# Kernel tuning notes

Measured on AMD Instinct MI355X. Metric: run time of the kernel, lower is better.

Reference implementation:

```python
import jax, jax.numpy as jnp
import numpy as np

TOP_K = 2
NUM_EXPERTS = 8
LB_COEFF = 0.01


def setup_inputs() -> dict:
    key = jax.random.key(0)
    ks = jax.random.split(key, 5)
    B, S, D, F, E = 4, 2048, 1024, 4096, NUM_EXPERTS
    s_in = 0.02
    return {
        "x": jax.random.normal(ks[0], (B, S, D), jnp.float32),
        "gate_w": jax.random.normal(ks[1], (D, E), jnp.float32) * s_in,
        "gate_b": jnp.zeros((E,), jnp.float32),
        "fc1_w": jax.random.normal(ks[2], (E, D, 2 * F), jnp.float32) * s_in,
        "fc1_b": jnp.zeros((E, 2 * F), jnp.float32),
        "fc2_w": jax.random.normal(ks[3], (E, F, D), jnp.float32) * s_in,
        "fc2_b": jnp.zeros((E, D), jnp.float32),
    }


def reference(x, gate_w, gate_b, fc1_w, fc1_b, fc2_w, fc2_b):
    B, S, D = x.shape
    E = gate_w.shape[1]
    xt = x.reshape(-1, D)                      # [T, D]
    T = xt.shape[0]

    gate_logits = xt @ gate_w + gate_b        # [T, E]
    gate_probs = jax.nn.softmax(gate_logits, axis=-1)
    top_w, top_i = jax.lax.top_k(gate_probs, TOP_K)      # [T, K]
    w_norm = top_w / (top_w.sum(-1, keepdims=True) + 1e-6)

    rows = jnp.arange(T)[:, None]
    # per-token per-expert combine weight (0 if expert not in top-k)
    combine = jnp.zeros((T, E), xt.dtype).at[rows, top_i].add(w_norm)  # [T, E]

    out = jnp.zeros_like(xt)
    for e in range(E):  # fixed small expert loop; each is a dense GEMM
        h = xt @ fc1_w[e] + fc1_b[e]                      # [T, 2F]
        a, g = jnp.split(h, 2, axis=-1)
        act = a * jax.nn.gelu(g, approximate=False)       # SwiGLU (exact gelu, torch default)
        y = act @ fc2_w[e] + fc2_b[e]                     # [T, D]
        out = out + combine[:, e:e + 1] * y

    chosen_mask = jnp.zeros((T, E), gate_probs.dtype).at[rows, top_i].set(1.0)
    frac = chosen_mask.mean(0)
    mean_probs = gate_probs.mean(0)
    lb_loss = LB_COEFF * E * jnp.sum(frac * mean_probs)

    return out.reshape(B, S, D), lb_loss
```

## Files before the change

### kernel.cpp

```cpp
#include <hip/hip_runtime.h>
#include <hip/hip_bf16.h>
#include <stdint.h>

typedef __attribute__((ext_vector_type(4))) float f32x4;
typedef __attribute__((ext_vector_type(16))) float f32x16;
typedef __attribute__((ext_vector_type(8))) __bf16 bf16x8;
typedef __attribute__((ext_vector_type(4))) unsigned short u16x4;
typedef unsigned short u16;

#define NTOK 8192
#define DDIM 1024
#define FDIM 4096
#define NEXP 8
#define NT1 144

#define WS_XB    0ull
#define WS_W1T   (16777216ull)
#define WS_W2T   (WS_W1T + 134217728ull)
#define WS_ACT   (WS_W2T + 67108864ull)
#define WS_LIST  (WS_ACT + 142606336ull)
#define WS_PAIRW (WS_LIST + 262144ull)
#define WS_CNT   (WS_PAIRW + 262144ull)
#define WS_SUMP  (WS_CNT + 32ull)
#define WS_PAD   (WS_SUMP + 32ull)
#define WS_OFF   (WS_PAD + 32ull)
#define WS_T1E   (WS_OFF + 32ull)
#define WS_T1R   (WS_T1E + 1024ull)
#define WS_SE    (WS_T1R + 1024ull)
#define WS_SP    (WS_SE + 65536ull)

static __device__ __forceinline__ u16 bf16rne(float f) {
  union { float f; uint32_t u; } c; c.f = f;
  return (u16)((c.u + 0x7FFFu + ((c.u >> 16) & 1u)) >> 16);
}

static __device__ __forceinline__ void load_lds16(const void* g, void* l) {
  __builtin_amdgcn_global_load_lds((const __attribute__((address_space(1))) void*)g,
                                   (__attribute__((address_space(3))) void*)l, 16, 0, 0);
}

__global__ __launch_bounds__(256) void gate_kernel(
    const float* __restrict__ x, const float* __restrict__ gw,
    const float* __restrict__ gb, u16* __restrict__ xb,
    int* __restrict__ cnt, float* __restrict__ sump,
    int* __restrict__ list, float* __restrict__ pairw,
    int* __restrict__ slotE, int* __restrict__ slotP) {
  const int tid = threadIdx.x;
  const int lane = tid & 63;
  const int wv = tid >> 6;
  const int t = blockIdx.x * 4 + wv;

  __shared__ float sp[8];
  if (tid < 8) sp[tid] = 0.f;
  __syncthreads();

  float acc[8] = {0.f,0.f,0.f,0.f,0.f,0.f,0.f,0.f};
  const float4* x4 = (const float4*)x + (size_t)t * 256;
  u16x4* xb4 = (u16x4*)xb + (size_t)t * 256;
  #pragma unroll
  for (int it = 0; it < 4; ++it) {
    const float4 xv = x4[it * 64 + lane];
    u16x4 bv;
    bv[0] = bf16rne(xv.x); bv[1] = bf16rne(xv.y);
    bv[2] = bf16rne(xv.z); bv[3] = bf16rne(xv.w);
    xb4[it * 64 + lane] = bv;
    const int d0 = (it * 64 + lane) * 4;
    #pragma unroll
    for (int j = 0; j < 4; ++j) {
      const float xs = (j == 0) ? xv.x : ((j == 1) ? xv.y : ((j == 2) ? xv.z : xv.w));
      const float* g = gw + (size_t)(d0 + j) * 8;
      #pragma unroll
      for (int e2 = 0; e2 < 8; ++e2) acc[e2] += xs * g[e2];
    }
  }
  #pragma unroll
  for (int e2 = 0; e2 < 8; ++e2) {
    float v = acc[e2];
    v += __shfl_xor(v, 1);  v += __shfl_xor(v, 2);  v += __shfl_xor(v, 4);
    v += __shfl_xor(v, 8);  v += __shfl_xor(v, 16); v += __shfl_xor(v, 32);
    acc[e2] = v;
  }
  float p[8]; float mx = -1e30f;
  #pragma unroll
  for (int e2 = 0; e2 < 8; ++e2) { p[e2] = acc[e2] + gb[e2]; mx = fmaxf(mx, p[e2]); }
  float s = 0.f;
  #pragma unroll
  for (int e2 = 0; e2 < 8; ++e2) { p[e2] = expf(p[e2] - mx); s += p[e2]; }
  const float inv = 1.f / s;
  #pragma unroll
  for (int e2 = 0; e2 < 8; ++e2) p[e2] *= inv;

  if (lane == 0) {
    int i1 = 0; float v1 = p[0];
    #pragma unroll
    for (int e2 = 1; e2 < 8; ++e2) if (p[e2] > v1) { v1 = p[e2]; i1 = e2; }
    int i2 = 0; float v2 = -1.f;
    #pragma unroll
    for (int e2 = 0; e2 < 8; ++e2) if (e2 != i1 && p[e2] > v2) { v2 = p[e2]; i2 = e2; }
    const float den = v1 + v2 + 1e-6f;
    const int p1 = atomicAdd(&cnt[i1], 1);
    list[i1 * NTOK + p1] = t; pairw[i1 * NTOK + p1] = v1 / den;
    slotE[2 * t] = i1; slotP[2 * t] = p1;
    const int p2 = atomicAdd(&cnt[i2], 1);
    list[i2 * NTOK + p2] = t; pairw[i2 * NTOK + p2] = v2 / den;
    slotE[2 * t + 1] = i2; slotP[2 * t + 1] = p2;
    #pragma unroll
    for (int e2 = 0; e2 < 8; ++e2) atomicAdd(&sp[e2], p[e2]);
  }
  __syncthreads();
  if (tid < 8) atomicAdd(&sump[tid], sp[tid]);
}

__global__ __launch_bounds__(256) void conv_transpose(
    const float* __restrict__ in, u16* __restrict__ out, int R, int C) {
  __shared__ float tile[64][65];
  const int e = blockIdx.z;
  const float* pin = in + (size_t)e * R * C;
  u16* pout = out + (size_t)e * R * C;
  const int tx = threadIdx.x & 15;
  const int ty = threadIdx.x >> 4;
  const int c0 = blockIdx.x * 64;
  const int r0 = blockIdx.y * 64;
  #pragma unroll
  for (int i = 0; i < 4; ++i) {
    const int r = ty + i * 16;
    const float4 v = *(const float4*)(pin + (size_t)(r0 + r) * C + c0 + tx * 4);
    tile[r][tx * 4 + 0] = v.x;
    tile[r][tx * 4 + 1] = v.y;
    tile[r][tx * 4 + 2] = v.z;
    tile[r][tx * 4 + 3] = v.w;
  }
  __syncthreads();
  #pragma unroll
  for (int i = 0; i < 4; ++i) {
    const int c = ty + i * 16;
    u16x4 o;
    o[0] = bf16rne(tile[tx * 4 + 0][c]);
    o[1] = bf16rne(tile[tx * 4 + 1][c]);
    o[2] = bf16rne(tile[tx * 4 + 2][c]);
    o[3] = bf16rne(tile[tx * 4 + 3][c]);
    *(u16x4*)(pout + (size_t)(c0 + c) * R + r0 + tx * 4) = o;
  }
}

__global__ void route_finalize(const int* __restrict__ cnt, const float* __restrict__ sump,
                               int* __restrict__ padc, int* __restrict__ offs,
                               int* __restrict__ list, float* __restrict__ pairw,
                               int* __restrict__ t1e, int* __restrict__ t1r,
                               float* __restrict__ lb_out) {
  __shared__ int s_c[8], s_p[8];
  const int tid = threadIdx.x;
  if (tid == 0) {
    int o = 0; float lb = 0.f;
    for (int e = 0; e < 8; ++e) {
      const int c = cnt[e];
      const int pc = (c + 127) & ~127;
      s_c[e] = c; s_p[e] = pc;
      padc[e] = pc; offs[e] = o; o += pc;
      lb += ((float)c / 8192.f) * (sump[e] / 8192.f);
    }
    lb_out[0] = 0.01f * 8.f * lb;
    int n1 = 0;
    for (int e = 0; e < 8; ++e)
      for (int r = 0; r < s_p[e]; r += 128) { t1e[n1] = e; t1r[n1] = r; ++n1; }
    for (; n1 < NT1; ++n1) { t1e[n1] = -1; t1r[n1] = 0; }
  }
  __syncthreads();
  for (int e = 0; e < 8; ++e)
    for (int pq = s_c[e] + tid; pq < s_p[e]; pq += blockDim.x) {
      list[e * NTOK + pq] = 0; pairw[e * NTOK + pq] = 0.f;
    }
}

__global__ __launch_bounds__(256) void gemm1_kernel(
    const u16* __restrict__ xb, const u16* __restrict__ w1t,
    const float* __restrict__ b1, const int* __restrict__ list,
    const int* __restrict__ offs,
    const int* __restrict__ t1e, const int* __restrict__ t1r,
    u16* __restrict__ act) {
  const int tt = blockIdx.y;
  const int e = t1e[tt];
  if (e < 0) return;
  const int row0 = t1r[tt];
  const int j = blockIdx.x;
  const int off_e = offs[e];

  __shared__ u16 lds[16384];

  const int tid = threadIdx.x;
  const int lane = tid & 63;
  const int wv = tid >> 6;
  const int wr = wv >> 1, wc = wv & 1;
  const int l31 = lane & 31, s5 = lane >> 5;

  const int rt = tid >> 2;
  const int ce = ((tid & 3) ^ ((rt >> 1) & 3)) * 8;
  const int tok0 = list[e * NTOK + row0 + rt];
  const int tok1 = list[e * NTOK + row0 + rt + 64];
  const u16* srcA0 = xb + (size_t)tok0 * DDIM + ce;
  const u16* srcA1 = xb + (size_t)tok1 * DDIM + ce;
  const int rB1 = rt + 64;
  const int gn0 = j * 64 + ((rt >> 6) & 1) * 32 + (rt & 31) + ((rt >> 5) & 1) * FDIM;
  const int gn1 = j * 64 + ((rB1 >> 6) & 1) * 32 + (rB1 & 31) + ((rB1 >> 5) & 1) * FDIM;
  const u16* srcB0 = w1t + ((size_t)e * 2 * FDIM + gn0) * DDIM + ce;
  const u16* srcB1 = w1t + ((size_t)e * 2 * FDIM + gn1) * DDIM + ce;

  const int xsw = (l31 >> 1) & 3;
  const int kel0 = (s5 ^ xsw) * 8;
  const int aB0 = (wr * 64 + l31) * 32 + kel0;  const int aB1 = aB0 ^ 16;
  const int bB0 = (wc * 64 + l31) * 32 + kel0;  const int bB1 = bB0 ^ 16;

  f32x16 acc[2][2];
  #pragma unroll
  for (int m = 0; m < 2; ++m)
    #pragma unroll
    for (int n = 0; n < 2; ++n)
      #pragma unroll
      for (int i = 0; i < 16; ++i) acc[m][n][i] = 0.f;

  #define STAGE1(buf, kt) do { \
    u16* _dA = &lds[(buf) * 4096 + wv * 512]; \
    u16* _dB = &lds[8192 + (buf) * 4096 + wv * 512]; \
    load_lds16(srcA0 + (kt) * 32, _dA); \
    load_lds16(srcA1 + (kt) * 32, _dA + 2048); \
    load_lds16(srcB0 + (kt) * 32, _dB); \
    load_lds16(srcB1 + (kt) * 32, _dB + 2048); \
  } while (0)

  STAGE1(0, 0);
  for (int kt = 0; kt < DDIM / 32; ++kt) {
    const int cur = kt & 1;
    __syncthreads();
    if (kt + 1 < DDIM / 32) STAGE1(cur ^ 1, kt + 1);
    const int bA = cur * 4096;
    const int bB = 8192 + cur * 4096;
    bf16x8 a0[2], a1[2], Bh0[2], Bh1[2];
    #pragma unroll
    for (int m = 0; m < 2; ++m) {
      a0[m] = *(const bf16x8*)&lds[bA + aB0 + m * 1024];
      a1[m] = *(const bf16x8*)&lds[bA + aB1 + m * 1024];
    }
    #pragma unroll
    for (int n = 0; n < 2; ++n) {
      Bh0[n] = *(const bf16x8*)&lds[bB + bB0 + n * 1024];
      Bh1[n] = *(const bf16x8*)&lds[bB + bB1 + n * 1024];
    }
    #pragma unroll
    for (int m = 0; m < 2; ++m)
      #pragma unroll
      for (int n = 0; n < 2; ++n) {
        acc[m][n] = __builtin_amdgcn_mfma_f32_32x32x16_bf16(a0[m], Bh0[n], acc[m][n], 0, 0, 0);
        acc[m][n] = __builtin_amdgcn_mfma_f32_32x32x16_bf16(a1[m], Bh1[n], acc[m][n], 0, 0, 0);
      }
  }
  #undef STAGE1

  const size_t actrow0 = (size_t)(off_e + row0);
  const int col = j * 64 + wc * 32 + l31;
  const float ba = b1[e * (2 * FDIM) + col];
  const float bg = b1[e * (2 * FDIM) + FDIM + col];
  #pragma unroll
  for (int m = 0; m < 2; ++m) {
    #pragma unroll
    for (int r = 0; r < 16; ++r) {
      const int row = wr * 64 + m * 32 + (r & 3) + 8 * (r >> 2) + 4 * s5;
      const float a = acc[m][0][r] + ba;
      const float g = acc[m][1][r] + bg;
      const float u2 = 1.5957691216057308f * (g + 0.044715f * g * g * g);
      const float sg = 1.f / (1.f + __expf(-u2));
      act[(actrow0 + row) * FDIM + col] = bf16rne(a * g * sg);
    }
  }
}

__global__ __launch_bounds__(256) void gemm2_kernel(
    const u16* __restrict__ act, const u16* __restrict__ w2t,
    const float* __restrict__ b2, const float* __restrict__ pairw,
    const int* __restrict__ offs,
    const int* __restrict__ t1e, const int* __restrict__ t1r,
    float* __restrict__ y) {
  const int bid = blockIdx.x;
  const int r8 = bid & 7;
  const int q = bid >> 3;
  const int jt = q & 7;
  const int tt = (q >> 3) * 8 + r8;
  const int e = t1e[tt];
  if (e < 0) return;
  const int row0 = t1r[tt];
  const int off_e = offs[e];

  __shared__ u16 lds[16384];

  const int tid = threadIdx.x;
  const int lane = tid & 63;
  const int wv = tid >> 6;
  const int wr = wv >> 1, wc = wv & 1;
  const int l31 = lane & 31, s5 = lane >> 5;

  const int rt = tid >> 2;
  const int ce = ((tid & 3) ^ ((rt >> 1) & 3)) * 8;
  const u16* srcA0 = act + (size_t)(off_e + row0 + rt) * FDIM + ce;
  const u16* srcA1 = act + (size_t)(off_e + row0 + rt + 64) * FDIM + ce;
  const u16* srcB0 = w2t + ((size_t)e * DDIM + jt * 128 + rt) * FDIM + ce;
  const u16* srcB1 = w2t + ((size_t)e * DDIM + jt * 128 + rt + 64) * FDIM + ce;

  const int xsw = (l31 >> 1) & 3;
  const int kel0 = (s5 ^ xsw) * 8;
  const int aB0 = (wr * 64 + l31) * 32 + kel0;  const int aB1 = aB0 ^ 16;
  const int bB0 = (wc * 64 + l31) * 32 + kel0;  const int bB1 = bB0 ^ 16;

  f32x16 acc[2][2];
  #pragma unroll
  for (int m = 0; m < 2; ++m)
    #pragma unroll
    for (int n = 0; n < 2; ++n)
      #pragma unroll
      for (int i = 0; i < 16; ++i) acc[m][n][i] = 0.f;

  #define STAGE2(buf, kt) do { \
    u16* _dA = &lds[(buf) * 4096 + wv * 512]; \
    u16* _dB = &lds[8192 + (buf) * 4096 + wv * 512]; \
    load_lds16(srcA0 + (kt) * 32, _dA); \
    load_lds16(srcA1 + (kt) * 32, _dA + 2048); \
    load_lds16(srcB0 + (kt) * 32, _dB); \
    load_lds16(srcB1 + (kt) * 32, _dB + 2048); \
  } while (0)

  STAGE2(0, 0);
  for (int kt = 0; kt < FDIM / 32; ++kt) {
    const int cur = kt & 1;
    __syncthreads();
    if (kt + 1 < FDIM / 32) STAGE2(cur ^ 1, kt + 1);
    const int bA = cur * 4096;
    const int bB = 8192 + cur * 4096;
    bf16x8 a0[2], a1[2], Bh0[2], Bh1[2];
    #pragma unroll
    for (int m = 0; m < 2; ++m) {
      a0[m] = *(const bf16x8*)&lds[bA + aB0 + m * 1024];
      a1[m] = *(const bf16x8*)&lds[bA + aB1 + m * 1024];
    }
    #pragma unroll
    for (int n = 0; n < 2; ++n) {
      Bh0[n] = *(const bf16x8*)&lds[bB + bB0 + n * 1024];
      Bh1[n] = *(const bf16x8*)&lds[bB + bB1 + n * 1024];
    }
    #pragma unroll
    for (int m = 0; m < 2; ++m)
      #pragma unroll
      for (int n = 0; n < 2; ++n) {
        acc[m][n] = __builtin_amdgcn_mfma_f32_32x32x16_bf16(a0[m], Bh0[n], acc[m][n], 0, 0, 0);
        acc[m][n] = __builtin_amdgcn_mfma_f32_32x32x16_bf16(a1[m], Bh1[n], acc[m][n], 0, 0, 0);
      }
  }
  #undef STAGE2

  #pragma unroll
  for (int m = 0; m < 2; ++m) {
    #pragma unroll
    for (int r = 0; r < 16; ++r) {
      const int row = wr * 64 + m * 32 + (r & 3) + 8 * (r >> 2) + 4 * s5;
      const int pos = row0 + row;
      const float pw = pairw[e * NTOK + pos];
      if (pw != 0.f) {
        float* yr = y + (size_t)(off_e + pos) * DDIM;
        #pragma unroll
        for (int n = 0; n < 2; ++n) {
          const int col = jt * 128 + wc * 64 + n * 32 + l31;
          yr[col] = (acc[m][n][r] + b2[e * DDIM + col]) * pw;
        }
      }
    }
  }
}

__global__ __launch_bounds__(256) void gather_kernel(
    const float* __restrict__ y, const int* __restrict__ slotE,
    const int* __restrict__ slotP, const int* __restrict__ offs,
    float* __restrict__ out) {
  const int t = blockIdx.x * 4 + (threadIdx.x >> 6);
  const int lane = threadIdx.x & 63;
  const int r1 = offs[slotE[2 * t]] + slotP[2 * t];
  const int r2 = offs[slotE[2 * t + 1]] + slotP[2 * t + 1];
  const float4* y1 = (const float4*)(y + (size_t)r1 * DDIM);
  const float4* y2 = (const float4*)(y + (size_t)r2 * DDIM);
  float4* o4 = (float4*)(out + (size_t)t * DDIM);
  #pragma unroll
  for (int i = 0; i < 4; ++i) {
    const float4 a = y1[i * 64 + lane];
    const float4 b = y2[i * 64 + lane];
    float4 r; r.x = a.x + b.x; r.y = a.y + b.y; r.z = a.z + b.z; r.w = a.w + b.w;
    o4[i * 64 + lane] = r;
  }
}

extern "C" void kernel_launch(void* const* d_in, const int* in_sizes, int n_in,
                              void* d_out, int out_size, void* d_ws, size_t ws_size,
                              hipStream_t stream) {
  const float* x   = (const float*)d_in[0];
  const float* gw  = (const float*)d_in[1];
  const float* gb  = (const float*)d_in[2];
  const float* f1w = (const float*)d_in[3];
  const float* f1b = (const float*)d_in[4];
  const float* f2w = (const float*)d_in[5];
  const float* f2b = (const float*)d_in[6];
  float* out = (float*)d_out;
  char* ws = (char*)d_ws;

  u16*   xb    = (u16*)(ws + WS_XB);
  u16*   w1t   = (u16*)(ws + WS_W1T);
  float* y     = (float*)(ws + WS_W1T);
  u16*   w2t   = (u16*)(ws + WS_W2T);
  u16*   act   = (u16*)(ws + WS_ACT);
  int*   list  = (int*)(ws + WS_LIST);
  float* pairw = (float*)(ws + WS_PAIRW);
  int*   cnt   = (int*)(ws + WS_CNT);
  float* sump  = (float*)(ws + WS_SUMP);
  int*   padc  = (int*)(ws + WS_PAD);
  int*   offs  = (int*)(ws + WS_OFF);
  int*   t1e   = (int*)(ws + WS_T1E);
  int*   t1r   = (int*)(ws + WS_T1R);
  int*   slotE = (int*)(ws + WS_SE);
  int*   slotP = (int*)(ws + WS_SP);

  (void)hipMemsetAsync(ws + WS_CNT, 0, 64, stream);

  gate_kernel<<<NTOK / 4, 256, 0, stream>>>(x, gw, gb, xb, cnt, sump, list, pairw, slotE, slotP);
  conv_transpose<<<dim3(8192 / 64, 1024 / 64, 8), 256, 0, stream>>>(f1w, w1t, 1024, 8192);
  conv_transpose<<<dim3(1024 / 64, 4096 / 64, 8), 256, 0, stream>>>(f2w, w2t, 4096, 1024);
  route_finalize<<<1, 256, 0, stream>>>(cnt, sump, padc, offs, list, pairw,
                                        t1e, t1r, out + 8388608);
  gemm1_kernel<<<dim3(64, NT1), 256, 0, stream>>>(xb, w1t, f1b, list, offs, t1e, t1r, act);
  gemm2_kernel<<<NT1 * 8, 256, 0, stream>>>(act, w2t, f2b, pairw, offs, t1e, t1r, y);
  gather_kernel<<<NTOK / 4, 256, 0, stream>>>(y, slotE, slotP, offs, out);
}
```

Measured before the change: 951.9 us.

## Narrow gemm2 tiles to 128x64, store expert outputs as bf16, simplify grid

The second expert GEMM drops from 128x128 to 128x64 output tiles with a 2D grid (16 x NT1), which doubles the block count, cuts LDS use, and halves accumulator registers so occupancy can rise. The grouped-tile block swizzle is removed in favour of plain blockIdx mapping. Per-expert outputs are now written as bf16 instead of fp32, and the gather kernel reads bf16 and converts before summing, halving intermediate traffic. In exchange the A tile is reloaded twice as often, L2 locality may drop without the swizzle, and bf16 rounding of the partial outputs adds precision error.

```diff
diff --git a/kernel.cpp b/kernel.cpp
--- a/kernel.cpp
+++ b/kernel.cpp
@@ -6,6 +6,7 @@
 typedef __attribute__((ext_vector_type(16))) float f32x16;
 typedef __attribute__((ext_vector_type(8))) __bf16 bf16x8;
 typedef __attribute__((ext_vector_type(4))) unsigned short u16x4;
+typedef __attribute__((ext_vector_type(8))) unsigned short u16x8;
 typedef unsigned short u16;
 
 #define NTOK 8192
@@ -32,6 +33,11 @@
 static __device__ __forceinline__ u16 bf16rne(float f) {
   union { float f; uint32_t u; } c; c.f = f;
   return (u16)((c.u + 0x7FFFu + ((c.u >> 16) & 1u)) >> 16);
+}
+
+static __device__ __forceinline__ float bf16tof(u16 v) {
+  union { uint32_t u; float f; } c; c.u = ((uint32_t)v) << 16;
+  return c.f;
 }
 
 static __device__ __forceinline__ void load_lds16(const void* g, void* l) {
@@ -278,18 +284,15 @@
     const float* __restrict__ b2, const float* __restrict__ pairw,
     const int* __restrict__ offs,
     const int* __restrict__ t1e, const int* __restrict__ t1r,
-    float* __restrict__ y) {
-  const int bid = blockIdx.x;
-  const int r8 = bid & 7;
-  const int q = bid >> 3;
-  const int jt = q & 7;
-  const int tt = (q >> 3) * 8 + r8;
+    u16* __restrict__ y) {
+  const int tt = blockIdx.y;
   const int e = t1e[tt];
   if (e < 0) return;
   const int row0 = t1r[tt];
+  const int jt = blockIdx.x;
   const int off_e = offs[e];
 
-  __shared__ u16 lds[16384];
+  __shared__ u16 lds[12288];
 
   const int tid = threadIdx.x;
   const int lane = tid & 63;
@@ -301,29 +304,25 @@
   const int ce = ((tid & 3) ^ ((rt >> 1) & 3)) * 8;
   const u16* srcA0 = act + (size_t)(off_e + row0 + rt) * FDIM + ce;
   const u16* srcA1 = act + (size_t)(off_e + row0 + rt + 64) * FDIM + ce;
-  const u16* srcB0 = w2t + ((size_t)e * DDIM + jt * 128 + rt) * FDIM + ce;
-  const u16* srcB1 = w2t + ((size_t)e * DDIM + jt * 128 + rt + 64) * FDIM + ce;
+  const u16* srcB0 = w2t + ((size_t)e * DDIM + jt * 64 + rt) * FDIM + ce;
 
   const int xsw = (l31 >> 1) & 3;
   const int kel0 = (s5 ^ xsw) * 8;
   const int aB0 = (wr * 64 + l31) * 32 + kel0;  const int aB1 = aB0 ^ 16;
-  const int bB0 = (wc * 64 + l31) * 32 + kel0;  const int bB1 = bB0 ^ 16;
-
-  f32x16 acc[2][2];
+  const int bB0 = (wc * 32 + l31) * 32 + kel0;  const int bB1 = bB0 ^ 16;
+
+  f32x16 acc[2];
   #pragma unroll
   for (int m = 0; m < 2; ++m)
     #pragma unroll
-    for (int n = 0; n < 2; ++n)
-      #pragma unroll
-      for (int i = 0; i < 16; ++i) acc[m][n][i] = 0.f;
+    for (int i = 0; i < 16; ++i) acc[m][i] = 0.f;
 
   #define STAGE2(buf, kt) do { \
     u16* _dA = &lds[(buf) * 4096 + wv * 512]; \
-    u16* _dB = &lds[8192 + (buf) * 4096 + wv * 512]; \
+    u16* _dB = &lds[8192 + (buf) * 2048 + wv * 512]; \
     load_lds16(srcA0 + (kt) * 32, _dA); \
     load_lds16(srcA1 + (kt) * 32, _dA + 2048); \
     load_lds16(srcB0 + (kt) * 32, _dB); \
-    load_lds16(srcB1 + (kt) * 32, _dB + 2048); \
   } while (0)
 
   STAGE2(0, 0);
@@ -332,28 +331,25 @@
     __syncthreads();
     if (kt + 1 < FDIM / 32) STAGE2(cur ^ 1, kt + 1);
     const int bA = cur * 4096;
-    const int bB = 8192 + cur * 4096;
-    bf16x8 a0[2], a1[2], Bh0[2], Bh1[2];
+    const int bB = 8192 + cur * 2048;
+    bf16x8 a0[2], a1[2], Bh0, Bh1;
     #pragma unroll
     for (int m = 0; m < 2; ++m) {
       a0[m] = *(const bf16x8*)&lds[bA + aB0 + m * 1024];
       a1[m] = *(const bf16x8*)&lds[bA + aB1 + m * 1024];
     }
-    #pragma unroll
-    for (int n = 0; n < 2; ++n) {
-      Bh0[n] = *(const bf16x8*)&lds[bB + bB0 + n * 1024];
-      Bh1[n] = *(const bf16x8*)&lds[bB + bB1 + n * 1024];
-    }
-    #pragma unroll
-    for (int m = 0; m < 2; ++m)
-      #pragma unroll
-      for (int n = 0; n < 2; ++n) {
-        acc[m][n] = __builtin_amdgcn_mfma_f32_32x32x16_bf16(a0[m], Bh0[n], acc[m][n], 0, 0, 0);
-        acc[m][n] = __builtin_amdgcn_mfma_f32_32x32x16_bf16(a1[m], Bh1[n], acc[m][n], 0, 0, 0);
-      }
+    Bh0 = *(const bf16x8*)&lds[bB + bB0];
+    Bh1 = *(const bf16x8*)&lds[bB + bB1];
+    #pragma unroll
+    for (int m = 0; m < 2; ++m) {
+      acc[m] = __builtin_amdgcn_mfma_f32_32x32x16_bf16(a0[m], Bh0, acc[m], 0, 0, 0);
+      acc[m] = __builtin_amdgcn_mfma_f32_32x32x16_bf16(a1[m], Bh1, acc[m], 0, 0, 0);
+    }
   }
   #undef STAGE2
 
+  const int col = jt * 64 + wc * 32 + l31;
+  const float bb = b2[e * DDIM + col];
   #pragma unroll
   for (int m = 0; m < 2; ++m) {
     #pragma unroll
@@ -362,34 +358,38 @@
       const int pos = row0 + row;
       const float pw = pairw[e * NTOK + pos];
       if (pw != 0.f) {
-        float* yr = y + (size_t)(off_e + pos) * DDIM;
-        #pragma unroll
-        for (int n = 0; n < 2; ++n) {
-          const int col = jt * 128 + wc * 64 + n * 32 + l31;
-          yr[col] = (acc[m][n][r] + b2[e * DDIM + col]) * pw;
-        }
+        y[(size_t)(off_e + pos) * DDIM + col] = bf16rne((acc[m][r] + bb) * pw);
       }
     }
   }
 }
 
 __global__ __launch_bounds__(256) void gather_kernel(
-    const float* __restrict__ y, const int* __restrict__ slotE,
+    const u16* __restrict__ y, const int* __restrict__ slotE,
     const int* __restrict__ slotP, const int* __restrict__ offs,
     float* __restrict__ out) {
   const int t = blockIdx.x * 4 + (threadIdx.x >> 6);
   const int lane = threadIdx.x & 63;
   const int r1 = offs[slotE[2 * t]] + slotP[2 * t];
   const int r2 = offs[slotE[2 * t + 1]] + slotP[2 * t + 1];
-  const float4* y1 = (const float4*)(y + (size_t)r1 * DDIM);
-  const float4* y2 = (const float4*)(y + (size_t)r2 * DDIM);
+  const u16x8* y1 = (const u16x8*)(y + (size_t)r1 * DDIM);
+  const u16x8* y2 = (const u16x8*)(y + (size_t)r2 * DDIM);
   float4* o4 = (float4*)(out + (size_t)t * DDIM);
   #pragma unroll
-  for (int i = 0; i < 4; ++i) {
-    const float4 a = y1[i * 64 + lane];
-    const float4 b = y2[i * 64 + lane];
-    float4 r; r.x = a.x + b.x; r.y = a.y + b.y; r.z = a.z + b.z; r.w = a.w + b.w;
-    o4[i * 64 + lane] = r;
+  for (int i = 0; i < 2; ++i) {
+    const u16x8 a = y1[i * 64 + lane];
+    const u16x8 b = y2[i * 64 + lane];
+    float4 r0, r1f;
+    r0.x = bf16tof(a[0]) + bf16tof(b[0]);
+    r0.y = bf16tof(a[1]) + bf16tof(b[1]);
+    r0.z = bf16tof(a[2]) + bf16tof(b[2]);
+    r0.w = bf16tof(a[3]) + bf16tof(b[3]);
+    r1f.x = bf16tof(a[4]) + bf16tof(b[4]);
+    r1f.y = bf16tof(a[5]) + bf16tof(b[5]);
+    r1f.z = bf16tof(a[6]) + bf16tof(b[6]);
+    r1f.w = bf16tof(a[7]) + bf16tof(b[7]);
+    o4[(i * 64 + lane) * 2]     = r0;
+    o4[(i * 64 + lane) * 2 + 1] = r1f;
   }
 }
 
@@ -408,7 +408,7 @@
 
   u16*   xb    = (u16*)(ws + WS_XB);
   u16*   w1t   = (u16*)(ws + WS_W1T);
-  float* y     = (float*)(ws + WS_W1T);
+  u16*   y     = (u16*)(ws + WS_W1T);
   u16*   w2t   = (u16*)(ws + WS_W2T);
   u16*   act   = (u16*)(ws + WS_ACT);
   int*   list  = (int*)(ws + WS_LIST);
@@ -430,6 +430,6 @@
   route_finalize<<<1, 256, 0, stream>>>(cnt, sump, padc, offs, list, pairw,
                                         t1e, t1r, out + 8388608);
   gemm1_kernel<<<dim3(64, NT1), 256, 0, stream>>>(xb, w1t, f1b, list, offs, t1e, t1r, act);
-  gemm2_kernel<<<NT1 * 8, 256, 0, stream>>>(act, w2t, f2b, pairw, offs, t1e, t1r, y);
+  gemm2_kernel<<<dim3(16, NT1), 256, 0, stream>>>(act, w2t, f2b, pairw, offs, t1e, t1r, y);
   gather_kernel<<<NTOK / 4, 256, 0, stream>>>(y, slotE, slotP, offs, out);
 }
```

Result: slower. 999.4 us (+5.0%).
